# Optimization experiments

Measured on AMD Instinct MI355X. Metric: run time of the kernel, lower is better.

The kernel has to match this reference:

```python
import math
import jax, jax.numpy as jnp
import numpy as np

IN_CH = 512
KEY = 512
VAL = 512
B, T = 8, 2048
SQRT_KEY = math.sqrt(float(KEY))


def setup_inputs() -> dict:
    key = jax.random.key(0)
    ks = jax.random.split(key, 7)
    s_in = 1.0 / math.sqrt(IN_CH)
    return {
        "x": jax.random.normal(ks[0], (B, T, IN_CH), dtype=jnp.float32),
        "Wq": jax.random.uniform(ks[1], (IN_CH, KEY), jnp.float32, -s_in, s_in),
        "bq": jax.random.uniform(ks[2], (KEY,), jnp.float32, -s_in, s_in),
        "Wk": jax.random.uniform(ks[3], (IN_CH, KEY), jnp.float32, -s_in, s_in),
        "bk": jax.random.uniform(ks[4], (KEY,), jnp.float32, -s_in, s_in),
        "Wv": jax.random.uniform(ks[5], (IN_CH, VAL), jnp.float32, -s_in, s_in),
        "bv": jax.random.uniform(ks[6], (VAL,), jnp.float32, -s_in, s_in),
    }


def reference(x, Wq, bq, Wk, bk, Wv, bv):
    # x: [B, T, C]
    q = x @ Wq + bq          # [B, T, K]
    k = x @ Wk + bk          # [B, T, K]
    v = x @ Wv + bv          # [B, T, V]
    logits = jnp.einsum("btk,bsk->bts", q, k)  # [B, T(q), T(kv)]
    mask = jnp.tril(jnp.ones((T, T), dtype=bool))  # causal: key s <= query t
    logits = jnp.where(mask[None, :, :], logits, -jnp.inf)
    # NOTE: original torch code softmaxes over dim=1 (the QUERY axis) — kept faithful.
    probs = jax.nn.softmax(logits / SQRT_KEY, axis=1)
    read = jnp.einsum("bts,bsv->btv", probs, v)  # [B, T, V]
    return jnp.concatenate((x, read), axis=2)    # [B, T, C+V]
```

## Files before the change

kernel.cpp:

```cpp
#include <hip/hip_runtime.h>
#include <hip/hip_bf16.h>
#include <math.h>

#define BATCH 8
#define SEQ   2048
#define CH    512
#define ROWS  (BATCH * SEQ)
#define INVSQ 0.044194173824159216f

#define BM 128
#define TP 68

typedef __attribute__((ext_vector_type(8))) __bf16 bf16x8;
typedef __attribute__((ext_vector_type(4))) float f32x4;

__device__ inline unsigned short f2bf(float f) {
    unsigned u = __builtin_bit_cast(unsigned, f);
    u += 0x7fffu + ((u >> 16) & 1u);
    return (unsigned short)(u >> 16);
}
__device__ inline float bf2f(unsigned short s) {
    unsigned u = ((unsigned)s) << 16;
    return __builtin_bit_cast(float, u);
}

__global__ __launch_bounds__(256) void fuse_x_kernel(
    const float* __restrict__ x, unsigned short* __restrict__ xb,
    float* __restrict__ out, float* __restrict__ Z)
{
    if (blockIdx.x < 64) Z[blockIdx.x * 256 + threadIdx.x] = 0.f;
    size_t base = ((size_t)blockIdx.x * 256 + threadIdx.x) * 8;
    size_t row = base >> 9, c = base & 511;
    float4 v0 = *(const float4*)(x + base);
    float4 v1 = *(const float4*)(x + base + 4);
    float* o = out + row * 1024 + c;
    *(float4*)o = v0;
    *(float4*)(o + 4) = v1;
    alignas(16) unsigned short t[8];
    t[0] = f2bf(v0.x); t[1] = f2bf(v0.y); t[2] = f2bf(v0.z); t[3] = f2bf(v0.w);
    t[4] = f2bf(v1.x); t[5] = f2bf(v1.y); t[6] = f2bf(v1.z); t[7] = f2bf(v1.w);
    *(uint4*)(xb + base) = *(const uint4*)t;
}

__global__ __launch_bounds__(256) void transpose_w_kernel(
    const float* __restrict__ Wq, const float* __restrict__ Wk,
    const float* __restrict__ Wv, unsigned short* __restrict__ Wt)
{
    __shared__ unsigned short T[64 * TP];
    const int k0 = blockIdx.x * 64, n0 = blockIdx.y * 64, w = blockIdx.z;
    const float* W = (w == 0) ? Wq : (w == 1) ? Wk : Wv;
    const int tid = threadIdx.x;
#pragma unroll
    for (int i = 0; i < 2; ++i) {
        int slot = tid + i * 256;
        int kr = slot >> 3, c8 = (slot & 7) << 3;
        float4 a = *(const float4*)(W + (size_t)(k0 + kr) * CH + n0 + c8);
        float4 b = *(const float4*)(W + (size_t)(k0 + kr) * CH + n0 + c8 + 4);
        T[(c8 + 0) * TP + kr] = f2bf(a.x); T[(c8 + 1) * TP + kr] = f2bf(a.y);
        T[(c8 + 2) * TP + kr] = f2bf(a.z); T[(c8 + 3) * TP + kr] = f2bf(a.w);
        T[(c8 + 4) * TP + kr] = f2bf(b.x); T[(c8 + 5) * TP + kr] = f2bf(b.y);
        T[(c8 + 6) * TP + kr] = f2bf(b.z); T[(c8 + 7) * TP + kr] = f2bf(b.w);
    }
    __syncthreads();
#pragma unroll
    for (int i = 0; i < 2; ++i) {
        int slot = tid + i * 256;
        int nr = slot >> 3, k8 = (slot & 7) << 3;
        uint2 lo = *(const uint2*)(T + nr * TP + k8);
        uint2 hi = *(const uint2*)(T + nr * TP + k8 + 4);
        uint4 u; u.x = lo.x; u.y = lo.y; u.z = hi.x; u.w = hi.y;
        *(uint4*)(Wt + ((size_t)w * CH + n0 + nr) * CH + k0 + k8) = u;
    }
}

__global__ __launch_bounds__(256) void transpose_v_kernel(
    const unsigned short* __restrict__ vb, const float* __restrict__ Z,
    unsigned short* __restrict__ Vt)
{
    __shared__ unsigned short T[64 * TP];
    const int s0 = blockIdx.x * 64, v0 = blockIdx.y * 64, b = blockIdx.z;
    const int tid = threadIdx.x;
#pragma unroll
    for (int i = 0; i < 2; ++i) {
        int slot = tid + i * 256;
        int sr = slot >> 3, c8 = (slot & 7) << 3;
        float inv = 1.0f / Z[b * SEQ + s0 + sr];
        uint4 raw = *(const uint4*)(vb + ((size_t)b * SEQ + s0 + sr) * CH + v0 + c8);
        const unsigned short* p = (const unsigned short*)&raw;
#pragma unroll
        for (int j = 0; j < 8; ++j)
            T[(c8 + j) * TP + sr] = f2bf(bf2f(p[j]) * inv);
    }
    __syncthreads();
#pragma unroll
    for (int i = 0; i < 2; ++i) {
        int slot = tid + i * 256;
        int vr = slot >> 3, s8 = (slot & 7) << 3;
        uint2 lo = *(const uint2*)(T + vr * TP + s8);
        uint2 hi = *(const uint2*)(T + vr * TP + s8 + 4);
        uint4 u; u.x = lo.x; u.y = lo.y; u.z = hi.x; u.w = hi.y;
        *(uint4*)(Vt + ((size_t)b * CH + v0 + vr) * SEQ + s0 + s8) = u;
    }
}

#define MFMA_ROW(r, af) \
    acc[r][0] = __builtin_amdgcn_mfma_f32_16x16x32_bf16(af, b0, acc[r][0], 0, 0, 0); \
    acc[r][1] = __builtin_amdgcn_mfma_f32_16x16x32_bf16(af, b1, acc[r][1], 0, 0, 0); \
    acc[r][2] = __builtin_amdgcn_mfma_f32_16x16x32_bf16(af, b2, acc[r][2], 0, 0, 0); \
    acc[r][3] = __builtin_amdgcn_mfma_f32_16x16x32_bf16(af, b3, acc[r][3], 0, 0, 0);

#define PIPELINE_LOOP                                                         \
    stageA(0); stageB(0); stageB(1);                                          \
    asm volatile("s_waitcnt vmcnt(2)" ::: "memory");                          \
    __builtin_amdgcn_s_barrier();                                             \
    __builtin_amdgcn_sched_barrier(0);                                        \
    _Pragma("unroll")                                                         \
    for (int U = 0; U < 16; ++U) {                                            \
        const unsigned short* Ab = lds + (U & 1) * 4096;                      \
        const unsigned short* Bb = lds + 8192 + (U & 1) * 8192;               \
        stageA(U + 1);                                                        \
        bf16x8 a0, a1, a2, a3, b0, b1, b2, b3;                                \
        b0 = *(const bf16x8*)(Bb + (brow +  0) * 32 + rswz);                  \
        b1 = *(const bf16x8*)(Bb + (brow + 16) * 32 + rswz);                  \
        b2 = *(const bf16x8*)(Bb + (brow + 32) * 32 + rswz);                  \
        b3 = *(const bf16x8*)(Bb + (brow + 48) * 32 + rswz);                  \
        a0 = *(const bf16x8*)(Ab + (arow +  0) * 32 + rswz);                  \
        a1 = *(const bf16x8*)(Ab + (arow + 16) * 32 + rswz);                  \
        a2 = *(const bf16x8*)(Ab + (arow + 32) * 32 + rswz);                  \
        a3 = *(const bf16x8*)(Ab + (arow + 48) * 32 + rswz);                  \
        asm volatile("s_waitcnt lgkmcnt(0)" ::: "memory");                    \
        __builtin_amdgcn_s_barrier();                                         \
        __builtin_amdgcn_sched_barrier(0);                                    \
        stageB(U + 2);                                                        \
        __builtin_amdgcn_s_setprio(1);                                        \
        MFMA_ROW(0, a0);                                                      \
        MFMA_ROW(1, a1);                                                      \
        MFMA_ROW(2, a2);                                                      \
        MFMA_ROW(3, a3);                                                      \
        __builtin_amdgcn_s_setprio(0);                                        \
        if (U <= 13)      asm volatile("s_waitcnt vmcnt(2)" ::: "memory");    \
        else if (U == 14) asm volatile("s_waitcnt vmcnt(0)" ::: "memory");    \
        __builtin_amdgcn_s_barrier();                                        \
        __builtin_amdgcn_sched_barrier(0);                                    \
    }

__global__ __launch_bounds__(512, 2) void qkv8_kernel(
    const unsigned short* __restrict__ xb, const unsigned short* __restrict__ Wt,
    const float* __restrict__ bq, const float* __restrict__ bk,
    const float* __restrict__ bv, unsigned short* __restrict__ qkv)
{
    __shared__ unsigned short lds[24576];
    const int tid = threadIdx.x;
    const int lane = tid & 63, wave = tid >> 6;
    const int waveA = wave >> 2;
    const int waveB = wave & 3;
    const int quad = lane >> 4, l16 = lane & 15;

    int id = (int)blockIdx.x;
    id = (id & 7) * 96 + (id >> 3);
    const int xt = id / 12, wt = id - xt * 12;
    const int xrow0 = xt << 8, wrow0 = wt << 7;

    const unsigned short* __restrict__ Wg = Wt + (size_t)wrow0 * CH;
    const unsigned short* __restrict__ Xg = xb + (size_t)xrow0 * CH;

    const int srow = tid >> 2;
    const int scol = (((tid & 3) ^ ((tid >> 3) & 3)) << 3);
    const size_t ga  = (size_t)srow * CH + scol;
    const size_t gb1 = (size_t)(srow + 128) * CH + scol;
    const int wdst = wave * 512;
    const int rswz = ((quad ^ ((l16 >> 1) & 3)) << 3);
    const int arow = waveA * 64 + l16;
    const int brow = waveB * 64 + l16;

    f32x4 acc[4][4] = {};

    auto stageA = [&](int V) {
        if (V >= 16) return;
        const unsigned short* g = Wg + ga + V * 32;
        unsigned short* d = lds + (V & 1) * 4096 + wdst;
        __builtin_amdgcn_global_load_lds(
            (const __attribute__((address_space(1))) unsigned int*)g,
            (__attribute__((address_space(3))) unsigned int*)d, 16, 0, 0);
    };
    auto stageB = [&](int V) {
        if (V >= 16) return;
        const unsigned short* g0 = Xg + ga + V * 32;
        const unsigned short* g1 = Xg + gb1 + V * 32;
        unsigned short* d = lds + 8192 + (V & 1) * 8192 + wdst;
        __builtin_amdgcn_global_load_lds(
            (const __attribute__((address_space(1))) unsigned int*)g0,
            (__attribute__((address_space(3))) unsigned int*)d, 16, 0, 0);
        __builtin_amdgcn_global_load_lds(
            (const __attribute__((address_space(1))) unsigned int*)g1,
            (__attribute__((address_space(3))) unsigned int*)(d + 4096), 16, 0, 0);
    };

    PIPELINE_LOOP

    const int which = wrow0 >> 9;
    const float* bias = (which == 0) ? bq : (which == 1) ? bk : bv;
    const float scale = (which == 0) ? INVSQ : 1.0f;
    unsigned short* outw = qkv + (size_t)which * ROWS * CH;
    const int colblk = wrow0 & 511;
#pragma unroll
    for (int r = 0; r < 4; ++r) {
        int colb = colblk + waveA * 64 + r * 16 + quad * 4;
        float4 b4 = *(const float4*)(bias + colb);
#pragma unroll
        for (int c = 0; c < 4; ++c) {
            int m = xrow0 + waveB * 64 + c * 16 + l16;
            alignas(8) unsigned short pk[4];
            pk[0] = f2bf((acc[r][c][0] + b4.x) * scale);
            pk[1] = f2bf((acc[r][c][1] + b4.y) * scale);
            pk[2] = f2bf((acc[r][c][2] + b4.z) * scale);
            pk[3] = f2bf((acc[r][c][3] + b4.w) * scale);
            *(uint2*)(outw + (size_t)m * CH + colb) = *(const uint2*)pk;
        }
    }
}

__global__ __launch_bounds__(512, 2) void logits8_kernel(
    const unsigned short* __restrict__ qb, const unsigned short* __restrict__ kb,
    unsigned short* __restrict__ E, float* __restrict__ Z)
{
    __shared__ unsigned short lds[24576];
    const int tid = threadIdx.x;
    const int lane = tid & 63, wave = tid >> 6;
    const int waveA = wave >> 2;
    const int waveB = wave & 3;
    const int quad = lane >> 4, l16 = lane & 15;

    const int b = (int)blockIdx.x & 7;
    const int i = (int)blockIdx.x >> 3;
    int tt2 = (int)((sqrtf(4.f * (float)i + 1.f) - 1.f) * 0.5f);
    int st = i - tt2 * (tt2 + 1);
    while (st < 0)           { --tt2; st = i - tt2 * (tt2 + 1); }
    while (st > 2 * tt2 + 1) { ++tt2; st = i - tt2 * (tt2 + 1); }
    const int m0s = st << 7;
    const int n0t = tt2 << 8;

    const unsigned short* __restrict__ Wg = kb + ((size_t)b * SEQ + m0s) * CH;
    const unsigned short* __restrict__ Xg = qb + ((size_t)b * SEQ + n0t) * CH;

    const int srow = tid >> 2;
    const int scol = (((tid & 3) ^ ((tid >> 3) & 3)) << 3);
    const size_t ga  = (size_t)srow * CH + scol;
    const size_t gb1 = (size_t)(srow + 128) * CH + scol;
    const int wdst = wave * 512;
    const int rswz = ((quad ^ ((l16 >> 1) & 3)) << 3);
    const int arow = waveA * 64 + l16;
    const int brow = waveB * 64 + l16;

    f32x4 acc[4][4] = {};

    auto stageA = [&](int V) {
        if (V >= 16) return;
        const unsigned short* g = Wg + ga + V * 32;
        unsigned short* d = lds + (V & 1) * 4096 + wdst;
        __builtin_amdgcn_global_load_lds(
            (const __attribute__((address_space(1))) unsigned int*)g,
            (__attribute__((address_space(3))) unsigned int*)d, 16, 0, 0);
    };
    auto stageB = [&](int V) {
        if (V >= 16) return;
        const unsigned short* g0 = Xg + ga + V * 32;
        const unsigned short* g1 = Xg + gb1 + V * 32;
        unsigned short* d = lds + 8192 + (V & 1) * 8192 + wdst;
        __builtin_amdgcn_global_load_lds(
            (const __attribute__((address_space(1))) unsigned int*)g0,
            (__attribute__((address_space(3))) unsigned int*)d, 16, 0, 0);
        __builtin_amdgcn_global_load_lds(
            (const __attribute__((address_space(1))) unsigned int*)g1,
            (__attribute__((address_space(3))) unsigned int*)(d + 4096), 16, 0, 0);
    };

    PIPELINE_LOOP

#pragma unroll
    for (int r = 0; r < 4; ++r) {
        int sb = m0s + waveA * 64 + r * 16 + quad * 4;
        float ev[4][4];
#pragma unroll
        for (int c = 0; c < 4; ++c) {
            int t = n0t + waveB * 64 + c * 16 + l16;
#pragma unroll
            for (int reg = 0; reg < 4; ++reg)
                ev[c][reg] = (sb + reg <= t) ? __expf(acc[r][c][reg]) : 0.f;
        }
#pragma unroll
        for (int reg = 0; reg < 4; ++reg) {
            float z = ev[0][reg] + ev[1][reg] + ev[2][reg] + ev[3][reg];
            z += __shfl_xor(z, 1);
            z += __shfl_xor(z, 2);
            z += __shfl_xor(z, 4);
            z += __shfl_xor(z, 8);
            if (l16 == 0) atomicAdd(&Z[b * SEQ + sb + reg], z);
        }
#pragma unroll
        for (int c = 0; c < 4; ++c) {
            int t = n0t + waveB * 64 + c * 16 + l16;
            alignas(8) unsigned short pk[4];
            pk[0] = f2bf(ev[c][0]); pk[1] = f2bf(ev[c][1]);
            pk[2] = f2bf(ev[c][2]); pk[3] = f2bf(ev[c][3]);
            *(uint2*)(E + ((size_t)b * SEQ + t) * SEQ + sb) = *(const uint2*)pk;
        }
    }
}
#undef PIPELINE_LOOP

__global__ __launch_bounds__(256, 2) void read8_kernel(
    const unsigned short* __restrict__ E, const unsigned short* __restrict__ Vt,
    float* __restrict__ out)
{
    __shared__ unsigned short lds[16384];
    const int tid = threadIdx.x;
    const int lane = tid & 63, wave = tid >> 6;
    const int waveA = wave >> 1;
    const int waveB = wave & 1;
    const int quad = lane >> 4, l16 = lane & 15;

    const int id = blockIdx.x;
    const int b = id & 7;
    const int rem = id >> 3;
    const int mv = rem & 3;
    const int r0 = rem >> 2;
    const int tt = (r0 < 8) ? r0 : 23 - r0;
    const int m0v = mv * BM;
    const int n0t = tt * BM;
    const int NT = (tt + 1) * 4;

    const unsigned short* __restrict__ Ag = Vt + ((size_t)b * CH + m0v) * SEQ;
    const unsigned short* __restrict__ Bg = E + ((size_t)b * SEQ + n0t) * SEQ;

    const int scol = (((lane & 3) ^ ((lane >> 3) & 3)) << 3);
    const int srow = wave * 16 + (lane >> 2);
    const size_t ga0 = (size_t)srow * SEQ + scol;
    const size_t ga1 = (size_t)(srow + 64) * SEQ + scol;
    const int wdst = wave * 512;
    const int rswz = ((quad ^ ((l16 >> 1) & 3)) << 3);
    const int arow = waveA * 64 + l16;
    const int brow = waveB * 64 + l16;

    f32x4 acc[4][4] = {};

    auto stageA = [&](int V) {
        if (V >= NT) return;
        const unsigned short* g0 = Ag + ga0 + V * 32;
        const unsigned short* g1 = Ag + ga1 + V * 32;
        unsigned short* d = lds + (V & 1) * 4096 + wdst;
        __builtin_amdgcn_global_load_lds(
            (const __attribute__((address_space(1))) unsigned int*)g0,
            (__attribute__((address_space(3))) unsigned int*)d, 16, 0, 0);
        __builtin_amdgcn_global_load_lds(
            (const __attribute__((address_space(1))) unsigned int*)g1,
            (__attribute__((address_space(3))) unsigned int*)(d + 2048), 16, 0, 0);
    };
    auto stageB = [&](int V) {
        if (V >= NT) return;
        const unsigned short* g0 = Bg + ga0 + V * 32;
        const unsigned short* g1 = Bg + ga1 + V * 32;
        unsigned short* d = lds + 8192 + (V & 1) * 4096 + wdst;
        __builtin_amdgcn_global_load_lds(
            (const __attribute__((address_space(1))) unsigned int*)g0,
            (__attribute__((address_space(3))) unsigned int*)d, 16, 0, 0);
        __builtin_amdgcn_global_load_lds(
            (const __attribute__((address_space(1))) unsigned int*)g1,
            (__attribute__((address_space(3))) unsigned int*)(d + 2048), 16, 0, 0);
    };

    stageA(0); stageB(0); stageB(1);
    asm volatile("s_waitcnt vmcnt(2)" ::: "memory");
    __builtin_amdgcn_s_barrier();
    __builtin_amdgcn_sched_barrier(0);

#pragma unroll 2
    for (int U = 0; U < NT; ++U) {
        const unsigned short* Ab = lds + (U & 1) * 4096;
        const unsigned short* Bb = lds + 8192 + (U & 1) * 4096;
        stageA(U + 1);
        bf16x8 a0, a1, a2, a3, b0, b1, b2, b3;
        b0 = *(const bf16x8*)(Bb + (brow +  0) * 32 + rswz);
        b1 = *(const bf16x8*)(Bb + (brow + 16) * 32 + rswz);
        b2 = *(const bf16x8*)(Bb + (brow + 32) * 32 + rswz);
        b3 = *(const bf16x8*)(Bb + (brow + 48) * 32 + rswz);
        a0 = *(const bf16x8*)(Ab + (arow +  0) * 32 + rswz);
        a1 = *(const bf16x8*)(Ab + (arow + 16) * 32 + rswz);
        a2 = *(const bf16x8*)(Ab + (arow + 32) * 32 + rswz);
        a3 = *(const bf16x8*)(Ab + (arow + 48) * 32 + rswz);
        asm volatile("s_waitcnt lgkmcnt(0)" ::: "memory");
        __builtin_amdgcn_s_barrier();
        __builtin_amdgcn_sched_barrier(0);
        stageB(U + 2);
        __builtin_amdgcn_s_setprio(1);
        MFMA_ROW(0, a0);
        MFMA_ROW(1, a1);
        MFMA_ROW(2, a2);
        MFMA_ROW(3, a3);
        __builtin_amdgcn_s_setprio(0);
        if (U <= NT - 3)      asm volatile("s_waitcnt vmcnt(2)" ::: "memory");
        else if (U == NT - 2) asm volatile("s_waitcnt vmcnt(0)" ::: "memory");
        __builtin_amdgcn_s_barrier();
        __builtin_amdgcn_sched_barrier(0);
    }

#pragma unroll
    for (int r = 0; r < 4; ++r) {
        int v = 512 + m0v + waveA * 64 + r * 16 + quad * 4;
#pragma unroll
        for (int c = 0; c < 4; ++c) {
            int t = n0t + waveB * 64 + c * 16 + l16;
            float4 f;
            f.x = acc[r][c][0]; f.y = acc[r][c][1];
            f.z = acc[r][c][2]; f.w = acc[r][c][3];
            *(float4*)(out + ((size_t)b * SEQ + t) * 1024 + v) = f;
        }
    }
}
#undef MFMA_ROW

extern "C" void kernel_launch(void* const* d_in, const int* in_sizes, int n_in,
                              void* d_out, int out_size, void* d_ws, size_t ws_size,
                              hipStream_t stream) {
    const float* x  = (const float*)d_in[0];
    const float* Wq = (const float*)d_in[1];
    const float* bq = (const float*)d_in[2];
    const float* Wk = (const float*)d_in[3];
    const float* bk = (const float*)d_in[4];
    const float* Wv = (const float*)d_in[5];
    const float* bv = (const float*)d_in[6];
    float* out = (float*)d_out;

    char* ws = (char*)d_ws;
    const size_t QKV_BYTES = (size_t)ROWS * CH * 2;
    const size_t E_BYTES   = (size_t)BATCH * SEQ * SEQ * 2;
    unsigned short* qkv = (unsigned short*)ws;
    unsigned short* qb = qkv;
    unsigned short* kb = (unsigned short*)(ws + QKV_BYTES);
    unsigned short* vb = (unsigned short*)(ws + 2 * QKV_BYTES);
    unsigned short* E  = (unsigned short*)(ws + 3 * QKV_BYTES);
    float* Z = (float*)(ws + 3 * QKV_BYTES + E_BYTES);
    unsigned short* xb = E;
    unsigned short* Wt = (unsigned short*)((char*)E + QKV_BYTES);
    unsigned short* Vt = qb;

    dim3 blk(256);
    fuse_x_kernel<<<dim3(4096), blk, 0, stream>>>(x, xb, out, Z);
    transpose_w_kernel<<<dim3(8, 8, 3), blk, 0, stream>>>(Wq, Wk, Wv, Wt);
    qkv8_kernel<<<dim3(768), dim3(512), 0, stream>>>(xb, Wt, bq, bk, bv, qkv);
    logits8_kernel<<<dim3(576), dim3(512), 0, stream>>>(qb, kb, E, Z);
    transpose_v_kernel<<<dim3(32, 8, 8), blk, 0, stream>>>(vb, Z, Vt);
    read8_kernel<<<dim3(512), blk, 0, stream>>>(E, Vt, out);
}
```

Measured before the change: 221.7 us.

## Use 128x128 tiles with K=64 steps and 4-wave blocks across GEMM kernels

The qkv and logits kernels switch from 512-thread blocks with 256x128 tiles to 256-thread blocks with 128x128 tiles. This doubles the grid and makes causal logits tiles 128-square. All three GEMM kernels now stage 64-wide K slices, which halves the pipeline iterations and barriers, with a new 8-way XOR swizzle and a shared pipeline macro. The aim is less per-step sync overhead, finer causal work granularity and better load balance. The cost is more LDS per block (64KB), which may lower occupancy, and less operand reuse per block in qkv.

```diff
diff --git a/kernel.cpp b/kernel.cpp
--- a/kernel.cpp
+++ b/kernel.cpp
@@ -8,7 +8,6 @@
 #define ROWS  (BATCH * SEQ)
 #define INVSQ 0.044194173824159216f
 
-#define BM 128
 #define TP 68
 
 typedef __attribute__((ext_vector_type(8))) __bf16 bf16x8;
@@ -103,100 +102,111 @@
     }
 }
 
-#define MFMA_ROW(r, af) \
-    acc[r][0] = __builtin_amdgcn_mfma_f32_16x16x32_bf16(af, b0, acc[r][0], 0, 0, 0); \
-    acc[r][1] = __builtin_amdgcn_mfma_f32_16x16x32_bf16(af, b1, acc[r][1], 0, 0, 0); \
-    acc[r][2] = __builtin_amdgcn_mfma_f32_16x16x32_bf16(af, b2, acc[r][2], 0, 0, 0); \
-    acc[r][3] = __builtin_amdgcn_mfma_f32_16x16x32_bf16(af, b3, acc[r][3], 0, 0, 0);
-
-#define PIPELINE_LOOP                                                         \
+#define FRAG_READS                                                            \
+    bf16x8 a0[4], a1[4], c0[4], c1[4];                                        \
+    _Pragma("unroll")                                                         \
+    for (int rr = 0; rr < 4; ++rr) {                                          \
+        const unsigned short* ap = Ab + (arow + rr * 16) * 64;                \
+        const unsigned short* bp = Bb + (brow + rr * 16) * 64;                \
+        a0[rr] = *(const bf16x8*)(ap + s80);                                  \
+        a1[rr] = *(const bf16x8*)(ap + s81);                                  \
+        c0[rr] = *(const bf16x8*)(bp + s80);                                  \
+        c1[rr] = *(const bf16x8*)(bp + s81);                                  \
+    }
+
+#define MFMA_TILE                                                             \
+    _Pragma("unroll")                                                         \
+    for (int rr = 0; rr < 4; ++rr)                                            \
+        _Pragma("unroll")                                                     \
+        for (int cc = 0; cc < 4; ++cc)                                        \
+            acc[rr][cc] = __builtin_amdgcn_mfma_f32_16x16x32_bf16(            \
+                a0[rr], c0[cc], acc[rr][cc], 0, 0, 0);                        \
+    _Pragma("unroll")                                                         \
+    for (int rr = 0; rr < 4; ++rr)                                            \
+        _Pragma("unroll")                                                     \
+        for (int cc = 0; cc < 4; ++cc)                                        \
+            acc[rr][cc] = __builtin_amdgcn_mfma_f32_16x16x32_bf16(            \
+                a1[rr], c1[cc], acc[rr][cc], 0, 0, 0);
+
+#define STAGE4(gsrc, dslab)                                                   \
+    _Pragma("unroll")                                                         \
+    for (int p = 0; p < 4; ++p)                                               \
+        __builtin_amdgcn_global_load_lds(                                     \
+            (const __attribute__((address_space(1))) unsigned int*)((gsrc) + (size_t)p * 32 * gstride), \
+            (__attribute__((address_space(3))) unsigned int*)((dslab) + p * 2048 + (tid << 3)), \
+            16, 0, 0);
+
+#define PIPE_PROLOGUE                                                         \
     stageA(0); stageB(0); stageB(1);                                          \
-    asm volatile("s_waitcnt vmcnt(2)" ::: "memory");                          \
+    asm volatile("s_waitcnt vmcnt(4)" ::: "memory");                          \
     __builtin_amdgcn_s_barrier();                                             \
-    __builtin_amdgcn_sched_barrier(0);                                        \
-    _Pragma("unroll")                                                         \
-    for (int U = 0; U < 16; ++U) {                                            \
-        const unsigned short* Ab = lds + (U & 1) * 4096;                      \
-        const unsigned short* Bb = lds + 8192 + (U & 1) * 8192;               \
+    __builtin_amdgcn_sched_barrier(0);
+
+#define PIPE_BODY(NTv)                                                        \
+    {                                                                         \
+        const unsigned short* Ab = lds + (U & 1) * 8192;                      \
+        const unsigned short* Bb = lds + 16384 + (U & 1) * 8192;              \
         stageA(U + 1);                                                        \
-        bf16x8 a0, a1, a2, a3, b0, b1, b2, b3;                                \
-        b0 = *(const bf16x8*)(Bb + (brow +  0) * 32 + rswz);                  \
-        b1 = *(const bf16x8*)(Bb + (brow + 16) * 32 + rswz);                  \
-        b2 = *(const bf16x8*)(Bb + (brow + 32) * 32 + rswz);                  \
-        b3 = *(const bf16x8*)(Bb + (brow + 48) * 32 + rswz);                  \
-        a0 = *(const bf16x8*)(Ab + (arow +  0) * 32 + rswz);                  \
-        a1 = *(const bf16x8*)(Ab + (arow + 16) * 32 + rswz);                  \
-        a2 = *(const bf16x8*)(Ab + (arow + 32) * 32 + rswz);                  \
-        a3 = *(const bf16x8*)(Ab + (arow + 48) * 32 + rswz);                  \
+        FRAG_READS                                                            \
         asm volatile("s_waitcnt lgkmcnt(0)" ::: "memory");                    \
         __builtin_amdgcn_s_barrier();                                         \
         __builtin_amdgcn_sched_barrier(0);                                    \
         stageB(U + 2);                                                        \
         __builtin_amdgcn_s_setprio(1);                                        \
-        MFMA_ROW(0, a0);                                                      \
-        MFMA_ROW(1, a1);                                                      \
-        MFMA_ROW(2, a2);                                                      \
-        MFMA_ROW(3, a3);                                                      \
+        MFMA_TILE                                                             \
         __builtin_amdgcn_s_setprio(0);                                        \
-        if (U <= 13)      asm volatile("s_waitcnt vmcnt(2)" ::: "memory");    \
-        else if (U == 14) asm volatile("s_waitcnt vmcnt(0)" ::: "memory");    \
-        __builtin_amdgcn_s_barrier();                                        \
+        if (U <= (NTv) - 3)      asm volatile("s_waitcnt vmcnt(4)" ::: "memory"); \
+        else if (U == (NTv) - 2) asm volatile("s_waitcnt vmcnt(0)" ::: "memory"); \
+        __builtin_amdgcn_s_barrier();                                         \
         __builtin_amdgcn_sched_barrier(0);                                    \
     }
 
-__global__ __launch_bounds__(512, 2) void qkv8_kernel(
+__global__ __launch_bounds__(256, 2) void qkv8_kernel(
     const unsigned short* __restrict__ xb, const unsigned short* __restrict__ Wt,
     const float* __restrict__ bq, const float* __restrict__ bk,
     const float* __restrict__ bv, unsigned short* __restrict__ qkv)
 {
-    __shared__ unsigned short lds[24576];
+    __shared__ unsigned short lds[32768];
     const int tid = threadIdx.x;
     const int lane = tid & 63, wave = tid >> 6;
-    const int waveA = wave >> 2;
-    const int waveB = wave & 3;
+    const int waveA = wave >> 1;
+    const int waveB = wave & 1;
     const int quad = lane >> 4, l16 = lane & 15;
 
     int id = (int)blockIdx.x;
-    id = (id & 7) * 96 + (id >> 3);
+    id = (id & 7) * 192 + (id >> 3);
     const int xt = id / 12, wt = id - xt * 12;
-    const int xrow0 = xt << 8, wrow0 = wt << 7;
-
+    const int xrow0 = xt << 7, wrow0 = wt << 7;
+
+    const size_t gstride = CH;
     const unsigned short* __restrict__ Wg = Wt + (size_t)wrow0 * CH;
     const unsigned short* __restrict__ Xg = xb + (size_t)xrow0 * CH;
 
-    const int srow = tid >> 2;
-    const int scol = (((tid & 3) ^ ((tid >> 3) & 3)) << 3);
-    const size_t ga  = (size_t)srow * CH + scol;
-    const size_t gb1 = (size_t)(srow + 128) * CH + scol;
-    const int wdst = wave * 512;
-    const int rswz = ((quad ^ ((l16 >> 1) & 3)) << 3);
+    const int scol = (((tid & 7) ^ ((tid >> 3) & 7)) << 3);
+    const size_t ga = (size_t)(tid >> 3) * gstride + scol;
+    const int s80 = ((quad ^ (l16 & 7)) << 3);
+    const int s81 = s80 ^ 32;
     const int arow = waveA * 64 + l16;
     const int brow = waveB * 64 + l16;
 
     f32x4 acc[4][4] = {};
 
     auto stageA = [&](int V) {
-        if (V >= 16) return;
-        const unsigned short* g = Wg + ga + V * 32;
-        unsigned short* d = lds + (V & 1) * 4096 + wdst;
-        __builtin_amdgcn_global_load_lds(
-            (const __attribute__((address_space(1))) unsigned int*)g,
-            (__attribute__((address_space(3))) unsigned int*)d, 16, 0, 0);
+        if (V >= 8) return;
+        const unsigned short* g = Wg + ga + V * 64;
+        unsigned short* d = lds + (V & 1) * 8192;
+        STAGE4(g, d)
     };
     auto stageB = [&](int V) {
-        if (V >= 16) return;
-        const unsigned short* g0 = Xg + ga + V * 32;
-        const unsigned short* g1 = Xg + gb1 + V * 32;
-        unsigned short* d = lds + 8192 + (V & 1) * 8192 + wdst;
-        __builtin_amdgcn_global_load_lds(
-            (const __attribute__((address_space(1))) unsigned int*)g0,
-            (__attribute__((address_space(3))) unsigned int*)d, 16, 0, 0);
-        __builtin_amdgcn_global_load_lds(
-            (const __attribute__((address_space(1))) unsigned int*)g1,
-            (__attribute__((address_space(3))) unsigned int*)(d + 4096), 16, 0, 0);
-    };
-
-    PIPELINE_LOOP
+        if (V >= 8) return;
+        const unsigned short* g = Xg + ga + V * 64;
+        unsigned short* d = lds + 16384 + (V & 1) * 8192;
+        STAGE4(g, d)
+    };
+
+    PIPE_PROLOGUE
+#pragma unroll
+    for (int U = 0; U < 8; ++U) PIPE_BODY(8)
 
     const int which = wrow0 >> 9;
     const float* bias = (which == 0) ? bq : (which == 1) ? bk : bv;
@@ -220,62 +230,55 @@
     }
 }
 
-__global__ __launch_bounds__(512, 2) void logits8_kernel(
+__global__ __launch_bounds__(256, 2) void logits8_kernel(
     const unsigned short* __restrict__ qb, const unsigned short* __restrict__ kb,
     unsigned short* __restrict__ E, float* __restrict__ Z)
 {
-    __shared__ unsigned short lds[24576];
+    __shared__ unsigned short lds[32768];
     const int tid = threadIdx.x;
     const int lane = tid & 63, wave = tid >> 6;
-    const int waveA = wave >> 2;
-    const int waveB = wave & 3;
+    const int waveA = wave >> 1;
+    const int waveB = wave & 1;
     const int quad = lane >> 4, l16 = lane & 15;
 
     const int b = (int)blockIdx.x & 7;
     const int i = (int)blockIdx.x >> 3;
-    int tt2 = (int)((sqrtf(4.f * (float)i + 1.f) - 1.f) * 0.5f);
-    int st = i - tt2 * (tt2 + 1);
-    while (st < 0)           { --tt2; st = i - tt2 * (tt2 + 1); }
-    while (st > 2 * tt2 + 1) { ++tt2; st = i - tt2 * (tt2 + 1); }
+    int tt = (int)((sqrtf(8.f * (float)i + 1.f) - 1.f) * 0.5f);
+    int st = i - ((tt * (tt + 1)) >> 1);
+    while (st < 0)  { --tt; st = i - ((tt * (tt + 1)) >> 1); }
+    while (st > tt) { ++tt; st = i - ((tt * (tt + 1)) >> 1); }
     const int m0s = st << 7;
-    const int n0t = tt2 << 8;
-
-    const unsigned short* __restrict__ Wg = kb + ((size_t)b * SEQ + m0s) * CH;
-    const unsigned short* __restrict__ Xg = qb + ((size_t)b * SEQ + n0t) * CH;
-
-    const int srow = tid >> 2;
-    const int scol = (((tid & 3) ^ ((tid >> 3) & 3)) << 3);
-    const size_t ga  = (size_t)srow * CH + scol;
-    const size_t gb1 = (size_t)(srow + 128) * CH + scol;
-    const int wdst = wave * 512;
-    const int rswz = ((quad ^ ((l16 >> 1) & 3)) << 3);
+    const int n0t = tt << 7;
+
+    const size_t gstride = CH;
+    const unsigned short* __restrict__ Ag = kb + ((size_t)b * SEQ + m0s) * CH;
+    const unsigned short* __restrict__ Bg = qb + ((size_t)b * SEQ + n0t) * CH;
+
+    const int scol = (((tid & 7) ^ ((tid >> 3) & 7)) << 3);
+    const size_t ga = (size_t)(tid >> 3) * gstride + scol;
+    const int s80 = ((quad ^ (l16 & 7)) << 3);
+    const int s81 = s80 ^ 32;
     const int arow = waveA * 64 + l16;
     const int brow = waveB * 64 + l16;
 
     f32x4 acc[4][4] = {};
 
     auto stageA = [&](int V) {
-        if (V >= 16) return;
-        const unsigned short* g = Wg + ga + V * 32;
-        unsigned short* d = lds + (V & 1) * 4096 + wdst;
-        __builtin_amdgcn_global_load_lds(
-            (const __attribute__((address_space(1))) unsigned int*)g,
-            (__attribute__((address_space(3))) unsigned int*)d, 16, 0, 0);
+        if (V >= 8) return;
+        const unsigned short* g = Ag + ga + V * 64;
+        unsigned short* d = lds + (V & 1) * 8192;
+        STAGE4(g, d)
     };
     auto stageB = [&](int V) {
-        if (V >= 16) return;
-        const unsigned short* g0 = Xg + ga + V * 32;
-        const unsigned short* g1 = Xg + gb1 + V * 32;
-        unsigned short* d = lds + 8192 + (V & 1) * 8192 + wdst;
-        __builtin_amdgcn_global_load_lds(
-            (const __attribute__((address_space(1))) unsigned int*)g0,
-            (__attribute__((address_space(3))) unsigned int*)d, 16, 0, 0);
-        __builtin_amdgcn_global_load_lds(
-            (const __attribute__((address_space(1))) unsigned int*)g1,
-            (__attribute__((address_space(3))) unsigned int*)(d + 4096), 16, 0, 0);
-    };
-
-    PIPELINE_LOOP
+        if (V >= 8) return;
+        const unsigned short* g = Bg + ga + V * 64;
+        unsigned short* d = lds + 16384 + (V & 1) * 8192;
+        STAGE4(g, d)
+    };
+
+    PIPE_PROLOGUE
+#pragma unroll
+    for (int U = 0; U < 8; ++U) PIPE_BODY(8)
 
 #pragma unroll
     for (int r = 0; r < 4; ++r) {
@@ -307,13 +310,12 @@
         }
     }
 }
-#undef PIPELINE_LOOP
 
 __global__ __launch_bounds__(256, 2) void read8_kernel(
     const unsigned short* __restrict__ E, const unsigned short* __restrict__ Vt,
     float* __restrict__ out)
 {
-    __shared__ unsigned short lds[16384];
+    __shared__ unsigned short lds[32768];
     const int tid = threadIdx.x;
     const int lane = tid & 63, wave = tid >> 6;
     const int waveA = wave >> 1;
@@ -326,19 +328,18 @@
     const int mv = rem & 3;
     const int r0 = rem >> 2;
     const int tt = (r0 < 8) ? r0 : 23 - r0;
-    const int m0v = mv * BM;
-    const int n0t = tt * BM;
-    const int NT = (tt + 1) * 4;
-
+    const int m0v = mv << 7;
+    const int n0t = tt << 7;
+    const int NT = (tt + 1) * 2;
+
+    const size_t gstride = SEQ;
     const unsigned short* __restrict__ Ag = Vt + ((size_t)b * CH + m0v) * SEQ;
     const unsigned short* __restrict__ Bg = E + ((size_t)b * SEQ + n0t) * SEQ;
 
-    const int scol = (((lane & 3) ^ ((lane >> 3) & 3)) << 3);
-    const int srow = wave * 16 + (lane >> 2);
-    const size_t ga0 = (size_t)srow * SEQ + scol;
-    const size_t ga1 = (size_t)(srow + 64) * SEQ + scol;
-    const int wdst = wave * 512;
-    const int rswz = ((quad ^ ((l16 >> 1) & 3)) << 3);
+    const int scol = (((tid & 7) ^ ((tid >> 3) & 7)) << 3);
+    const size_t ga = (size_t)(tid >> 3) * gstride + scol;
+    const int s80 = ((quad ^ (l16 & 7)) << 3);
+    const int s81 = s80 ^ 32;
     const int arow = waveA * 64 + l16;
     const int brow = waveB * 64 + l16;
 
@@ -346,63 +347,20 @@
 
     auto stageA = [&](int V) {
         if (V >= NT) return;
-        const unsigned short* g0 = Ag + ga0 + V * 32;
-        const unsigned short* g1 = Ag + ga1 + V * 32;
-        unsigned short* d = lds + (V & 1) * 4096 + wdst;
-        __builtin_amdgcn_global_load_lds(
-            (const __attribute__((address_space(1))) unsigned int*)g0,
-            (__attribute__((address_space(3))) unsigned int*)d, 16, 0, 0);
-        __builtin_amdgcn_global_load_lds(
-            (const __attribute__((address_space(1))) unsigned int*)g1,
-            (__attribute__((address_space(3))) unsigned int*)(d + 2048), 16, 0, 0);
+        const unsigned short* g = Ag + ga + V * 64;
+        unsigned short* d = lds + (V & 1) * 8192;
+        STAGE4(g, d)
     };
     auto stageB = [&](int V) {
         if (V >= NT) return;
-        const unsigned short* g0 = Bg + ga0 + V * 32;
-        const unsigned short* g1 = Bg + ga1 + V * 32;
-        unsigned short* d = lds + 8192 + (V & 1) * 4096 + wdst;
-        __builtin_amdgcn_global_load_lds(
-            (const __attribute__((address_space(1))) unsigned int*)g0,
-            (__attribute__((address_space(3))) unsigned int*)d, 16, 0, 0);
-        __builtin_amdgcn_global_load_lds(
-            (const __attribute__((address_space(1))) unsigned int*)g1,
-            (__attribute__((address_space(3))) unsigned int*)(d + 2048), 16, 0, 0);
-    };
-
-    stageA(0); stageB(0); stageB(1);
-    asm volatile("s_waitcnt vmcnt(2)" ::: "memory");
-    __builtin_amdgcn_s_barrier();
-    __builtin_amdgcn_sched_barrier(0);
-
+        const unsigned short* g = Bg + ga + V * 64;
+        unsigned short* d = lds + 16384 + (V & 1) * 8192;
+        STAGE4(g, d)
+    };
+
+    PIPE_PROLOGUE
 #pragma unroll 2
-    for (int U = 0; U < NT; ++U) {
-        const unsigned short* Ab = lds + (U & 1) * 4096;
-        const unsigned short* Bb = lds + 8192 + (U & 1) * 4096;
-        stageA(U + 1);
-        bf16x8 a0, a1, a2, a3, b0, b1, b2, b3;
-        b0 = *(const bf16x8*)(Bb + (brow +  0) * 32 + rswz);
-        b1 = *(const bf16x8*)(Bb + (brow + 16) * 32 + rswz);
-        b2 = *(const bf16x8*)(Bb + (brow + 32) * 32 + rswz);
-        b3 = *(const bf16x8*)(Bb + (brow + 48) * 32 + rswz);
-        a0 = *(const bf16x8*)(Ab + (arow +  0) * 32 + rswz);
-        a1 = *(const bf16x8*)(Ab + (arow + 16) * 32 + rswz);
-        a2 = *(const bf16x8*)(Ab + (arow + 32) * 32 + rswz);
-        a3 = *(const bf16x8*)(Ab + (arow + 48) * 32 + rswz);
-        asm volatile("s_waitcnt lgkmcnt(0)" ::: "memory");
-        __builtin_amdgcn_s_barrier();
-        __builtin_amdgcn_sched_barrier(0);
-        stageB(U + 2);
-        __builtin_amdgcn_s_setprio(1);
-        MFMA_ROW(0, a0);
-        MFMA_ROW(1, a1);
-        MFMA_ROW(2, a2);
-        MFMA_ROW(3, a3);
-        __builtin_amdgcn_s_setprio(0);
-        if (U <= NT - 3)      asm volatile("s_waitcnt vmcnt(2)" ::: "memory");
-        else if (U == NT - 2) asm volatile("s_waitcnt vmcnt(0)" ::: "memory");
-        __builtin_amdgcn_s_barrier();
-        __builtin_amdgcn_sched_barrier(0);
-    }
+    for (int U = 0; U < NT; ++U) PIPE_BODY(NT)
 
 #pragma unroll
     for (int r = 0; r < 4; ++r) {
@@ -417,7 +375,6 @@
         }
     }
 }
-#undef MFMA_ROW
 
 extern "C" void kernel_launch(void* const* d_in, const int* in_sizes, int n_in,
                               void* d_out, int out_size, void* d_ws, size_t ws_size,
@@ -447,8 +404,8 @@
     dim3 blk(256);
     fuse_x_kernel<<<dim3(4096), blk, 0, stream>>>(x, xb, out, Z);
     transpose_w_kernel<<<dim3(8, 8, 3), blk, 0, stream>>>(Wq, Wk, Wv, Wt);
-    qkv8_kernel<<<dim3(768), dim3(512), 0, stream>>>(xb, Wt, bq, bk, bv, qkv);
-    logits8_kernel<<<dim3(576), dim3(512), 0, stream>>>(qb, kb, E, Z);
+    qkv8_kernel<<<dim3(1536), blk, 0, stream>>>(xb, Wt, bq, bk, bv, qkv);
+    logits8_kernel<<<dim3(1088), blk, 0, stream>>>(qb, kb, E, Z);
     transpose_v_kernel<<<dim3(32, 8, 8), blk, 0, stream>>>(vb, Z, Vt);
     read8_kernel<<<dim3(512), blk, 0, stream>>>(E, Vt, out);
 }
```

Result: faster. 213.9 us (-3.5%).
